# Kernel tuning notes

Hardware: AMD Instinct MI355X
Metric: run time of the kernel (lower is better)

Reference implementation:

```python
import jax, jax.numpy as jnp
import numpy as np

H, C = 4, 32
NT, NDAT, NDEV = 50000, 20000, 4
EDT, EVT, ETT = 800000, 200000, 400000


def _gat_conv(xs, xd, src, dst, ea, Ws, Wd, We, As, Ad, Ae, b, n_dst, concat):
    # linear projections -> [N, H, C]
    hs = (xs @ Ws).reshape(-1, H, C)
    hd = (xd @ Wd).reshape(-1, H, C)
    he = (ea @ We).reshape(-1, H, C)
    # per-edge attention logits [E, H]
    al = (hs * As).sum(-1)[src] + (hd * Ad).sum(-1)[dst] + (he * Ae).sum(-1)
    al = jax.nn.leaky_relu(al, 0.2)
    # segment softmax over incoming edges of each dst node
    amax = jax.ops.segment_max(al, dst, num_segments=n_dst)
    amax = jnp.where(jnp.isfinite(amax), amax, 0.0)
    ex = jnp.exp(al - amax[dst])
    den = jax.ops.segment_sum(ex, dst, num_segments=n_dst)
    w = ex / (den[dst] + 1e-16)
    # weighted scatter-add of source messages
    out = jax.ops.segment_sum(hs[src] * w[..., None], dst, num_segments=n_dst)
    out = out.reshape(n_dst, H * C) if concat else out.mean(axis=1)
    return out + b


def _add_self_loops_mean(src, dst, ea, n):
    # PyG add_self_loops(fill_value='mean'): loop edge_attr = mean of incoming edge_attr per node
    cnt = jax.ops.segment_sum(jnp.ones(dst.shape, ea.dtype), dst, num_segments=n)
    ea_mean = jax.ops.segment_sum(ea, dst, num_segments=n) / jnp.maximum(cnt, 1.0)[:, None]
    loops = jnp.arange(n, dtype=src.dtype)
    return (jnp.concatenate([src, loops]), jnp.concatenate([dst, loops]),
            jnp.concatenate([ea, ea_mean], axis=0))


def setup_inputs() -> dict:
    key = jax.random.key(0)
    ks = iter(jax.random.split(key, 40))
    nrm = lambda shape, fan: jax.random.normal(next(ks), shape, jnp.float32) / np.sqrt(fan)
    inp = {}
    inp['x_data'] = jax.random.normal(next(ks), (NDAT, 8), jnp.float32)
    inp['x_tasks'] = jax.random.normal(next(ks), (NT, 16), jnp.float32)
    inp['x_dev'] = jax.random.normal(next(ks), (NDEV, 8), jnp.float32)
    inp['ei_dt'] = jnp.stack([jax.random.randint(next(ks), (EDT,), 0, NDAT),
                              jax.random.randint(next(ks), (EDT,), 0, NT)]).astype(jnp.int32)
    inp['ea_dt'] = jax.random.normal(next(ks), (EDT, 8), jnp.float32)
    inp['ei_vt'] = jnp.stack([jax.random.randint(next(ks), (EVT,), 0, NDEV),
                              jax.random.randint(next(ks), (EVT,), 0, NT)]).astype(jnp.int32)
    inp['ea_vt'] = jax.random.normal(next(ks), (EVT, 6), jnp.float32)
    inp['ei_tt'] = jnp.stack([jax.random.randint(next(ks), (ETT,), 0, NT),
                              jax.random.randint(next(ks), (ETT,), 0, NT)]).astype(jnp.int32)
    inp['ea_tt'] = jax.random.normal(next(ks), (ETT, 4), jnp.float32)
    # conv1: (data -> tasks), concat=True
    inp['Ws1'] = nrm((8, H * C), 8); inp['Wd1'] = nrm((16, H * C), 16); inp['We1'] = nrm((8, H * C), 8)
    inp['As1'] = nrm((H, C), C); inp['Ad1'] = nrm((H, C), C); inp['Ae1'] = nrm((H, C), C)
    inp['b1'] = jnp.zeros((H * C,), jnp.float32)
    # conv2: (devices -> tasks), concat=True
    inp['Ws2'] = nrm((8, H * C), 8); inp['Wd2'] = nrm((16, H * C), 16); inp['We2'] = nrm((6, H * C), 6)
    inp['As2'] = nrm((H, C), C); inp['Ad2'] = nrm((H, C), C); inp['Ae2'] = nrm((H, C), C)
    inp['b2'] = jnp.zeros((H * C,), jnp.float32)
    # conv3: tasks -> tasks, single lin (256 -> H*C), concat=False, self loops
    inp['W3'] = nrm((2 * H * C, H * C), 2 * H * C); inp['We3'] = nrm((4, H * C), 4)
    inp['As3'] = nrm((H, C), C); inp['Ad3'] = nrm((H, C), C); inp['Ae3'] = nrm((H, C), C)
    inp['b3'] = jnp.zeros((C,), jnp.float32)
    return inp


def reference(x_data, x_tasks, x_dev, ei_dt, ea_dt, ei_vt, ea_vt, ei_tt, ea_tt,
              Ws1, Wd1, We1, As1, Ad1, Ae1, b1,
              Ws2, Wd2, We2, As2, Ad2, Ae2, b2,
              W3, We3, As3, Ad3, Ae3, b3):
    t_data = jax.nn.relu(_gat_conv(x_data, x_tasks, ei_dt[0], ei_dt[1], ea_dt,
                                   Ws1, Wd1, We1, As1, Ad1, Ae1, b1, NT, True))
    t_dev = jax.nn.relu(_gat_conv(x_dev, x_tasks, ei_vt[0], ei_vt[1], ea_vt,
                                  Ws2, Wd2, We2, As2, Ad2, Ae2, b2, NT, True))
    tasks = jnp.concatenate([t_data, t_dev], axis=1)  # [NT, 256]
    src, dst, ea = _add_self_loops_mean(ei_tt[0], ei_tt[1], ea_tt, NT)
    x = _gat_conv(tasks, tasks, src, dst, ea, W3, W3, We3, As3, Ad3, Ae3, b3, NT, False)
    x = jax.nn.relu(x)
    # dropout(p=0.5) is identity in eval mode
    return x
```

## Files before the change

kernel.cpp:

```cpp
#include <hip/hip_runtime.h>
#include <math.h>

static const int NT = 50000, NDAT = 20000, NDEV = 4;
static const int EDT = 800000, EVT = 200000, ETT = 400000;

static const int SCAN_TILE = 2048, SCAN_NB = 25;

static const int HT   = EDT + EVT + ETT;
static const int IN_A = HT + NDAT * 128;
static const int IN_B = IN_A + NDAT * 4;
static const int IN_C = IN_B + NT * 4;
static const int IN_D = IN_C + NDEV * 128;
static const int IN_E = IN_D + NDEV * 4;
static const int IN_F = IN_E + 256 * 128;
static const int FRONT_N = IN_F;

static const size_t OFF_TASKS = 0;
static const size_t OFF_HS    = 12800000;
static const size_t OFF_RANK  = OFF_HS;
static const size_t OFF_HSB1  = OFF_HS + 1400000;
static const size_t OFF_REC1  = OFF_HS + 2680000;
static const size_t OFF_HSB3  = OFF_HS;
static const size_t OFF_REC2  = 19200000;
static const size_t OFF_REC3  = 20000000;
static const size_t OFF_DEG   = 23200000;
static const size_t OFF_RP    = 23350000;
static const size_t OFF_AS1   = 23500004;
static const size_t OFF_AD1   = 23580004;
static const size_t OFF_AD2   = 23780004;
static const size_t OFF_HS2   = 23980004;
static const size_t OFF_AS2   = 23980516;
static const size_t OFF_QS1   = 23980532;
static const size_t OFF_QD1   = 23980564;
static const size_t OFF_P1    = 23980628;
static const size_t OFF_QS2   = 23980660;
static const size_t OFF_QD2   = 23980692;
static const size_t OFF_P2    = 23980756;
static const size_t OFF_P3    = 23980780;
static const size_t OFF_BSUM  = 23980796;
static const size_t OFF_W3HT  = 23980924;
static const size_t OFF_W3LT  = 23997308;
static const size_t WS_TOTAL  = 24013692;

typedef short v8s __attribute__((ext_vector_type(8)));
typedef float v4f __attribute__((ext_vector_type(4)));

__device__ __forceinline__ float lrelu(float a) { return a > 0.f ? a : 0.2f * a; }
__device__ __forceinline__ unsigned short f2bf(float x) {
    unsigned int u = __float_as_uint(x);
    return (unsigned short)((u + 0x7FFFu + ((u >> 16) & 1u)) >> 16);
}
__device__ __forceinline__ float bf2f(unsigned short h) {
    return __uint_as_float(((unsigned int)h) << 16);
}
__device__ __forceinline__ float bfsel(unsigned int lo01, unsigned int lo23, int h) {
    unsigned int word = (h < 2) ? lo01 : lo23;
    return bf2f((unsigned short)((h & 1) ? (word >> 16) : (word & 0xFFFFu)));
}
__device__ __forceinline__ void cvt_split(const float4& A, const float4& B, v8s& hi, v8s& lo) {
    union { unsigned short u[8]; v8s v; } H, L;
    float f[8] = {A.x, A.y, A.z, A.w, B.x, B.y, B.z, B.w};
    #pragma unroll
    for (int i = 0; i < 8; ++i) {
        unsigned short h = f2bf(f[i]);
        H.u[i] = h;
        L.u[i] = f2bf(f[i] - bf2f(h));
    }
    hi = H.v; lo = L.v;
}

__global__ void k_proj_small(const float* Ws1, const float* As1,
                             const float* Wd1, const float* Ad1,
                             const float* We1, const float* Ae1,
                             const float* Ws2, const float* As2,
                             const float* Wd2, const float* Ad2,
                             const float* We2, const float* Ae2,
                             const float* We3, const float* Ae3,
                             float* Qs1, float* Qd1, float* P1,
                             float* Qs2, float* Qd2, float* P2, float* P3) {
    int t = threadIdx.x;
    const float *W, *A; float* O; int u;
    if      (t < 32)  { W = Ws1; A = As1; O = Qs1; u = t; }
    else if (t < 96)  { W = Wd1; A = Ad1; O = Qd1; u = t - 32; }
    else if (t < 128) { W = We1; A = Ae1; O = P1;  u = t - 96; }
    else if (t < 160) { W = Ws2; A = As2; O = Qs2; u = t - 128; }
    else if (t < 224) { W = Wd2; A = Ad2; O = Qd2; u = t - 160; }
    else if (t < 248) { W = We2; A = Ae2; O = P2;  u = t - 224; }
    else if (t < 264) { W = We3; A = Ae3; O = P3;  u = t - 248; }
    else return;
    int k = u >> 2, h = u & 3;
    float acc = 0.f;
    for (int c = 0; c < 32; ++c) acc += W[k * 128 + h * 32 + c] * A[h * 32 + c];
    O[k * 4 + h] = acc;
}

__global__ __launch_bounds__(256) void k_front(const float* __restrict__ x_data,
                                               const float* __restrict__ Ws1,
                                               unsigned short* __restrict__ hsb1,
                                               const float* __restrict__ Qs1,
                                               float* __restrict__ as1,
                                               const float* __restrict__ x_tasks,
                                               const float* __restrict__ Qd1,
                                               const float* __restrict__ Qd2,
                                               float* __restrict__ ad1, float* __restrict__ ad2,
                                               const float* __restrict__ x_dev,
                                               const float* __restrict__ Ws2,
                                               float* __restrict__ hs2,
                                               const float* __restrict__ Qs2,
                                               float* __restrict__ as2,
                                               const float* __restrict__ W3,
                                               unsigned short* __restrict__ w3hT,
                                               unsigned short* __restrict__ w3lT,
                                               const int* __restrict__ dt,
                                               const int* __restrict__ vt,
                                               const int* __restrict__ tt,
                                               int* __restrict__ deg,
                                               int* __restrict__ rank) {
    int idx = blockIdx.x * blockDim.x + threadIdx.x;
    if (idx < HT) {
        if (idx < EDT)
            rank[idx] = atomicAdd(&deg[dt[EDT + idx]], 1);
        else if (idx < EDT + EVT)
            rank[idx] = atomicAdd(&deg[NT + vt[EVT + (idx - EDT)]], 1);
        else
            rank[idx] = atomicAdd(&deg[2 * NT + tt[ETT + (idx - EDT - EVT)]], 1);
    } else if (idx < IN_A) {
        int i = idx - HT;
        int n = i >> 7, j = i & 127;
        float acc = 0.f;
        #pragma unroll
        for (int k = 0; k < 8; ++k) acc += x_data[n * 8 + k] * Ws1[k * 128 + j];
        hsb1[i] = f2bf(acc);
    } else if (idx < IN_B) {
        int i = idx - IN_A;
        int n = i >> 2, h = i & 3;
        float acc = 0.f;
        #pragma unroll
        for (int k = 0; k < 8; ++k) acc += x_data[n * 8 + k] * Qs1[k * 4 + h];
        as1[i] = acc;
    } else if (idx < IN_C) {
        int i = idx - IN_B;
        int n = i >> 2, h = i & 3;
        float a = 0.f, b = 0.f;
        #pragma unroll
        for (int k = 0; k < 16; ++k) {
            float v = x_tasks[n * 16 + k];
            a += v * Qd1[k * 4 + h];
            b += v * Qd2[k * 4 + h];
        }
        ad1[i] = a; ad2[i] = b;
    } else if (idx < IN_D) {
        int i = idx - IN_C;
        int n = i >> 7, j = i & 127;
        float acc = 0.f;
        #pragma unroll
        for (int k = 0; k < 8; ++k) acc += x_dev[n * 8 + k] * Ws2[k * 128 + j];
        hs2[i] = acc;
    } else if (idx < IN_E) {
        int i = idx - IN_D;
        int n = i >> 2, h = i & 3;
        float acc = 0.f;
        #pragma unroll
        for (int k = 0; k < 8; ++k) acc += x_dev[n * 8 + k] * Qs2[k * 4 + h];
        as2[i] = acc;
    } else if (idx < IN_F) {
        int i = idx - IN_E;
        int k = i >> 7, n = i & 127;
        float x = W3[i];
        unsigned short h = f2bf(x);
        w3hT[n * 256 + k] = h;
        w3lT[n * 256 + k] = f2bf(x - bf2f(h));
    }
}

__global__ __launch_bounds__(256) void k_scan_part(const int* __restrict__ deg,
                                                   int* __restrict__ bsum) {
    int b = blockIdx.x;
    int g = b / SCAN_NB, t = b % SCAN_NB;
    int base = t * SCAN_TILE + threadIdx.x * 8;
    const int* dg = deg + (size_t)g * NT;
    int s = 0;
    if (base + 8 <= NT) {
        int4 a = *reinterpret_cast<const int4*>(dg + base);
        int4 c = *reinterpret_cast<const int4*>(dg + base + 4);
        s = a.x + a.y + a.z + a.w + c.x + c.y + c.z + c.w;
    } else {
        for (int i = 0; i < 8; ++i) if (base + i < NT) s += dg[base + i];
    }
    __shared__ int red[256];
    red[threadIdx.x] = s;
    __syncthreads();
    for (int off = 128; off > 0; off >>= 1) {
        if (threadIdx.x < off) red[threadIdx.x] += red[threadIdx.x + off];
        __syncthreads();
    }
    if (threadIdx.x == 0) bsum[b] = red[0];
}

__global__ __launch_bounds__(256) void k_scan_final(const int* __restrict__ deg,
                                                    const int* __restrict__ bsum,
                                                    int* __restrict__ rp) {
    int b = blockIdx.x;
    int g = b / SCAN_NB, t = b % SCAN_NB;
    int tid = threadIdx.x;
    int base = t * SCAN_TILE + tid * 8;
    const int* dg = deg + (size_t)g * NT;
    int* rpg = rp + (size_t)g * (NT + 1);
    int v[8];
    int s = 0;
    if (base + 8 <= NT) {
        int4 a = *reinterpret_cast<const int4*>(dg + base);
        int4 c = *reinterpret_cast<const int4*>(dg + base + 4);
        v[0] = a.x; v[1] = a.y; v[2] = a.z; v[3] = a.w;
        v[4] = c.x; v[5] = c.y; v[6] = c.z; v[7] = c.w;
        s = v[0] + v[1] + v[2] + v[3] + v[4] + v[5] + v[6] + v[7];
    } else {
        #pragma unroll
        for (int i = 0; i < 8; ++i) {
            v[i] = (base + i < NT) ? dg[base + i] : 0;
            s += v[i];
        }
    }
    __shared__ int sums[256];
    sums[tid] = s;
    __syncthreads();
    for (int off = 1; off < 256; off <<= 1) {
        int x = (tid >= off) ? sums[tid - off] : 0;
        __syncthreads();
        sums[tid] += x;
        __syncthreads();
    }
    int toff = 0;
    for (int t2 = 0; t2 < t; ++t2) toff += bsum[g * SCAN_NB + t2];
    int run = toff + (tid ? sums[tid - 1] : 0);
    #pragma unroll
    for (int i = 0; i < 8; ++i) {
        int idx = base + i;
        if (idx < NT) {
            rpg[idx] = run; run += v[i];
            if (idx == NT - 1) rpg[NT] = run;
        }
    }
}

__global__ void k_permute_w(const int* __restrict__ dt, const int* __restrict__ vt,
                            const int* __restrict__ tt, const int* __restrict__ rank,
                            const int* __restrict__ rp,
                            const float* __restrict__ as1, const float* __restrict__ ad1,
                            const float* __restrict__ P1, const float* __restrict__ ea1,
                            const float* __restrict__ as2, const float* __restrict__ ad2,
                            const float* __restrict__ P2, const float* __restrict__ ea2,
                            const float* __restrict__ P3, const float* __restrict__ ea3,
                            uint4* __restrict__ rec1, uint4* __restrict__ rec2,
                            uint4* __restrict__ rec3) {
    int e = blockIdx.x * blockDim.x + threadIdx.x;
    if (e < EDT) {
        int s = dt[e], d = dt[EDT + e];
        int slot = rp[d] + rank[e];
        float l[4];
        #pragma unroll
        for (int h = 0; h < 4; ++h) l[h] = as1[s * 4 + h] + ad1[d * 4 + h];
        float4 A = *reinterpret_cast<const float4*>(&ea1[(size_t)e * 8]);
        float4 B = *reinterpret_cast<const float4*>(&ea1[(size_t)e * 8 + 4]);
        float ev[8] = {A.x, A.y, A.z, A.w, B.x, B.y, B.z, B.w};
        #pragma unroll
        for (int k = 0; k < 8; ++k)
            #pragma unroll
            for (int h = 0; h < 4; ++h) l[h] += ev[k] * P1[k * 4 + h];
        unsigned int w01 = (unsigned int)f2bf(expf(lrelu(l[0])))
                         | ((unsigned int)f2bf(expf(lrelu(l[1]))) << 16);
        unsigned int w23 = (unsigned int)f2bf(expf(lrelu(l[2])))
                         | ((unsigned int)f2bf(expf(lrelu(l[3]))) << 16);
        rec1[slot] = make_uint4(w01, w23, (unsigned int)s, 0u);
    } else if (e < EDT + EVT) {
        int ee = e - EDT;
        int s = vt[ee], d = vt[EVT + ee];
        int slot = rp[(NT + 1) + d] + rank[e];
        float l[4];
        #pragma unroll
        for (int h = 0; h < 4; ++h) l[h] = as2[s * 4 + h] + ad2[d * 4 + h];
        float2 a = *reinterpret_cast<const float2*>(&ea2[(size_t)ee * 6]);
        float2 b = *reinterpret_cast<const float2*>(&ea2[(size_t)ee * 6 + 2]);
        float2 c = *reinterpret_cast<const float2*>(&ea2[(size_t)ee * 6 + 4]);
        float ev[6] = {a.x, a.y, b.x, b.y, c.x, c.y};
        #pragma unroll
        for (int k = 0; k < 6; ++k)
            #pragma unroll
            for (int h = 0; h < 4; ++h) l[h] += ev[k] * P2[k * 4 + h];
        unsigned int w01 = (unsigned int)f2bf(expf(lrelu(l[0])))
                         | ((unsigned int)f2bf(expf(lrelu(l[1]))) << 16);
        unsigned int w23 = (unsigned int)f2bf(expf(lrelu(l[2])))
                         | ((unsigned int)f2bf(expf(lrelu(l[3]))) << 16);
        rec2[slot] = make_uint4(w01, w23, (unsigned int)s, 0u);
    } else if (e < EDT + EVT + ETT) {
        int ee = e - EDT - EVT;
        int s = tt[ee], d = tt[ETT + ee];
        int slot = rp[2 * (NT + 1) + d] + rank[e];
        float4 q = *reinterpret_cast<const float4*>(&ea3[(size_t)ee * 4]);
        float ae[4];
        #pragma unroll
        for (int h = 0; h < 4; ++h)
            ae[h] = q.x * P3[h] + q.y * P3[4 + h] + q.z * P3[8 + h] + q.w * P3[12 + h];
        unsigned int a01 = (unsigned int)f2bf(ae[0]) | ((unsigned int)f2bf(ae[1]) << 16);
        unsigned int a23 = (unsigned int)f2bf(ae[2]) | ((unsigned int)f2bf(ae[3]) << 16);
        rec3[slot] = make_uint4((unsigned int)s, a01, a23, 0u);
    }
}

__global__ __launch_bounds__(256) void k_gather12(const int* __restrict__ rp1,
                                                  const uint4* __restrict__ rec1,
                                                  const unsigned short* __restrict__ hsb,
                                                  const float* __restrict__ b1,
                                                  const int* __restrict__ rp2,
                                                  const uint4* __restrict__ rec2,
                                                  const float* __restrict__ hs2,
                                                  const float* __restrict__ b2,
                                                  float* __restrict__ tasks) {
    int tid = threadIdx.x;
    int lane = tid & 31;
    int h = lane >> 3;
    if (blockIdx.x < NT / 8) {
        int d = blockIdx.x * 8 + (tid >> 5);
        int c0 = (lane & 7) * 4;
        int i0 = rp1[d], i1 = rp1[d + 1];
        float a0 = 0.f, a1 = 0.f, a2 = 0.f, a3 = 0.f, den = 0.f;
        int i = i0;
        for (; i + 4 <= i1; i += 4) {
            uint4 r0 = rec1[i], r1 = rec1[i + 1], r2 = rec1[i + 2], r3 = rec1[i + 3];
            float w0 = bfsel(r0.x, r0.y, h);
            float w1 = bfsel(r1.x, r1.y, h);
            float w2 = bfsel(r2.x, r2.y, h);
            float w3 = bfsel(r3.x, r3.y, h);
            ushort4 m0 = *reinterpret_cast<const ushort4*>(&hsb[(size_t)r0.z * 128 + h * 32 + c0]);
            ushort4 m1 = *reinterpret_cast<const ushort4*>(&hsb[(size_t)r1.z * 128 + h * 32 + c0]);
            ushort4 m2 = *reinterpret_cast<const ushort4*>(&hsb[(size_t)r2.z * 128 + h * 32 + c0]);
            ushort4 m3 = *reinterpret_cast<const ushort4*>(&hsb[(size_t)r3.z * 128 + h * 32 + c0]);
            a0 += w0 * bf2f(m0.x) + w1 * bf2f(m1.x) + w2 * bf2f(m2.x) + w3 * bf2f(m3.x);
            a1 += w0 * bf2f(m0.y) + w1 * bf2f(m1.y) + w2 * bf2f(m2.y) + w3 * bf2f(m3.y);
            a2 += w0 * bf2f(m0.z) + w1 * bf2f(m1.z) + w2 * bf2f(m2.z) + w3 * bf2f(m3.z);
            a3 += w0 * bf2f(m0.w) + w1 * bf2f(m1.w) + w2 * bf2f(m2.w) + w3 * bf2f(m3.w);
            den += w0 + w1 + w2 + w3;
        }
        for (; i < i1; ++i) {
            uint4 r = rec1[i];
            float w = bfsel(r.x, r.y, h);
            ushort4 m = *reinterpret_cast<const ushort4*>(&hsb[(size_t)r.z * 128 + h * 32 + c0]);
            a0 += w * bf2f(m.x); a1 += w * bf2f(m.y);
            a2 += w * bf2f(m.z); a3 += w * bf2f(m.w);
            den += w;
        }
        int j0 = h * 32 + c0;
        float4 b4 = *reinterpret_cast<const float4*>(&b1[j0]);
        float r = 1.f / (den + 1e-16f);
        float4 o = make_float4(fmaxf(a0 * r + b4.x, 0.f), fmaxf(a1 * r + b4.y, 0.f),
                               fmaxf(a2 * r + b4.z, 0.f), fmaxf(a3 * r + b4.w, 0.f));
        *reinterpret_cast<float4*>(&tasks[(size_t)d * 256 + j0]) = o;
    } else {
        int d = (blockIdx.x - NT / 8) * 8 + (tid >> 5);
        int i0 = rp2[d], i1 = rp2[d + 1];
        float ax = 0.f, ay = 0.f, az = 0.f, aw = 0.f, den = 0.f;
        int i = i0;
        for (; i + 4 <= i1; i += 4) {
            uint4 r0 = rec2[i], r1 = rec2[i + 1], r2 = rec2[i + 2], r3 = rec2[i + 3];
            float w0 = bfsel(r0.x, r0.y, h);
            float w1 = bfsel(r1.x, r1.y, h);
            float w2 = bfsel(r2.x, r2.y, h);
            float w3 = bfsel(r3.x, r3.y, h);
            float4 v0 = *reinterpret_cast<const float4*>(&hs2[r0.z * 128 + lane * 4]);
            float4 v1 = *reinterpret_cast<const float4*>(&hs2[r1.z * 128 + lane * 4]);
            float4 v2 = *reinterpret_cast<const float4*>(&hs2[r2.z * 128 + lane * 4]);
            float4 v3 = *reinterpret_cast<const float4*>(&hs2[r3.z * 128 + lane * 4]);
            ax += v0.x * w0 + v1.x * w1 + v2.x * w2 + v3.x * w3;
            ay += v0.y * w0 + v1.y * w1 + v2.y * w2 + v3.y * w3;
            az += v0.z * w0 + v1.z * w1 + v2.z * w2 + v3.z * w3;
            aw += v0.w * w0 + v1.w * w1 + v2.w * w2 + v3.w * w3;
            den += w0 + w1 + w2 + w3;
        }
        for (; i < i1; ++i) {
            uint4 r4 = rec2[i];
            float w = bfsel(r4.x, r4.y, h);
            float4 v = *reinterpret_cast<const float4*>(&hs2[r4.z * 128 + lane * 4]);
            ax += v.x * w; ay += v.y * w; az += v.z * w; aw += v.w * w;
            den += w;
        }
        float4 b4 = *reinterpret_cast<const float4*>(&b2[lane * 4]);
        float r = 1.f / (den + 1e-16f);
        float4 o = make_float4(fmaxf(ax * r + b4.x, 0.f), fmaxf(ay * r + b4.y, 0.f),
                               fmaxf(az * r + b4.z, 0.f), fmaxf(aw * r + b4.w, 0.f));
        *reinterpret_cast<float4*>(&tasks[(size_t)d * 256 + 128 + lane * 4]) = o;
    }
}

__global__ __launch_bounds__(256) void k_gather_c3(const int* __restrict__ rp,
                                                   const uint4* __restrict__ rec,
                                                   const float* __restrict__ as3,
                                                   const float* __restrict__ ad3,
                                                   const unsigned short* __restrict__ hsb,
                                                   const float* __restrict__ b3,
                                                   float* __restrict__ out) {
    int tid = threadIdx.x;
    int d = blockIdx.x * 8 + (tid >> 5);
    int lane = tid & 31;
    int h = lane >> 3;
    int c0 = (lane & 7) * 4;
    float adv = ad3[d * 4 + h];
    int i0 = rp[d], i1 = rp[d + 1];
    float a0 = 0.f, a1 = 0.f, a2 = 0.f, a3 = 0.f, den = 0.f, aes = 0.f;
    int i = i0;
    for (; i + 4 <= i1; i += 4) {
        uint4 r0 = rec[i], r1 = rec[i + 1], r2 = rec[i + 2], r3 = rec[i + 3];
        float s0 = as3[(size_t)r0.x * 4 + h], s1 = as3[(size_t)r1.x * 4 + h];
        float s2 = as3[(size_t)r2.x * 4 + h], s3 = as3[(size_t)r3.x * 4 + h];
        ushort4 m0 = *reinterpret_cast<const ushort4*>(&hsb[(size_t)r0.x * 128 + h * 32 + c0]);
        ushort4 m1 = *reinterpret_cast<const ushort4*>(&hsb[(size_t)r1.x * 128 + h * 32 + c0]);
        ushort4 m2 = *reinterpret_cast<const ushort4*>(&hsb[(size_t)r2.x * 128 + h * 32 + c0]);
        ushort4 m3 = *reinterpret_cast<const ushort4*>(&hsb[(size_t)r3.x * 128 + h * 32 + c0]);
        float ae0 = bfsel(r0.y, r0.z, h);
        float ae1 = bfsel(r1.y, r1.z, h);
        float ae2 = bfsel(r2.y, r2.z, h);
        float ae3 = bfsel(r3.y, r3.z, h);
        float w0 = expf(lrelu(s0 + adv + ae0));
        float w1 = expf(lrelu(s1 + adv + ae1));
        float w2 = expf(lrelu(s2 + adv + ae2));
        float w3 = expf(lrelu(s3 + adv + ae3));
        a0 += w0 * bf2f(m0.x) + w1 * bf2f(m1.x) + w2 * bf2f(m2.x) + w3 * bf2f(m3.x);
        a1 += w0 * bf2f(m0.y) + w1 * bf2f(m1.y) + w2 * bf2f(m2.y) + w3 * bf2f(m3.y);
        a2 += w0 * bf2f(m0.z) + w1 * bf2f(m1.z) + w2 * bf2f(m2.z) + w3 * bf2f(m3.z);
        a3 += w0 * bf2f(m0.w) + w1 * bf2f(m1.w) + w2 * bf2f(m2.w) + w3 * bf2f(m3.w);
        den += w0 + w1 + w2 + w3;
        aes += ae0 + ae1 + ae2 + ae3;
    }
    for (; i < i1; ++i) {
        uint4 r4 = rec[i];
        float s = as3[(size_t)r4.x * 4 + h];
        ushort4 m = *reinterpret_cast<const ushort4*>(&hsb[(size_t)r4.x * 128 + h * 32 + c0]);
        float ae = bfsel(r4.y, r4.z, h);
        float w = expf(lrelu(s + adv + ae));
        a0 += w * bf2f(m.x); a1 += w * bf2f(m.y);
        a2 += w * bf2f(m.z); a3 += w * bf2f(m.w);
        den += w; aes += ae;
    }
    float cnt = (float)(i1 - i0);
    float mloop = aes / fmaxf(cnt, 1.f);
    float exl = expf(lrelu(as3[(size_t)d * 4 + h] + adv + mloop));
    ushort4 md = *reinterpret_cast<const ushort4*>(&hsb[(size_t)d * 128 + h * 32 + c0]);
    float rden = 1.f / (den + exl + 1e-16f);
    float p0 = (a0 + exl * bf2f(md.x)) * rden;
    float p1 = (a1 + exl * bf2f(md.y)) * rden;
    float p2 = (a2 + exl * bf2f(md.z)) * rden;
    float p3 = (a3 + exl * bf2f(md.w)) * rden;
    p0 += __shfl_xor(p0, 8, 32); p0 += __shfl_xor(p0, 16, 32);
    p1 += __shfl_xor(p1, 8, 32); p1 += __shfl_xor(p1, 16, 32);
    p2 += __shfl_xor(p2, 8, 32); p2 += __shfl_xor(p2, 16, 32);
    p3 += __shfl_xor(p3, 8, 32); p3 += __shfl_xor(p3, 16, 32);
    if ((lane >> 3) == 0) {
        float4 o;
        o.x = fmaxf(0.25f * p0 + b3[c0 + 0], 0.f);
        o.y = fmaxf(0.25f * p1 + b3[c0 + 1], 0.f);
        o.z = fmaxf(0.25f * p2 + b3[c0 + 2], 0.f);
        o.w = fmaxf(0.25f * p3 + b3[c0 + 3], 0.f);
        *reinterpret_cast<float4*>(&out[(size_t)d * 32 + c0]) = o;
    }
}

__global__ __launch_bounds__(256, 2) void k_gemm_mfma(const float* __restrict__ T,
                                                      const unsigned short* __restrict__ w3hT,
                                                      const unsigned short* __restrict__ w3lT,
                                                      const float* __restrict__ As3,
                                                      const float* __restrict__ Ad3,
                                                      unsigned short* __restrict__ hsb,
                                                      float* __restrict__ as3o,
                                                      float* __restrict__ ad3o) {
    __shared__ uint4 sB[2][2048];
    int tid = threadIdx.x;
    int lane = tid & 63;
    int arow = lane & 15;
    int kgrp = lane >> 4;
    int s0 = blockIdx.x * 8 + (tid >> 6) * 2;
    int ss0 = s0 < 3125 ? s0 : 3124;
    int ss1 = (s0 + 1) < 3125 ? (s0 + 1) : 3124;
    const uint4* w3h4 = reinterpret_cast<const uint4*>(w3hT);
    const uint4* w3l4 = reinterpret_cast<const uint4*>(w3lT);

    v4f acc[2][8];
    #pragma unroll
    for (int sp = 0; sp < 2; ++sp)
        #pragma unroll
        for (int nt = 0; nt < 8; ++nt) acc[sp][nt] = (v4f)0.f;

    #pragma unroll
    for (int kt = 0; kt < 2; ++kt) {
        __syncthreads();
        float4 a0[8], a1[8];
        const float* Ta0 = T + (size_t)(ss0 * 16 + arow) * 256 + kt * 128 + kgrp * 8;
        const float* Ta1 = T + (size_t)(ss1 * 16 + arow) * 256 + kt * 128 + kgrp * 8;
        #pragma unroll
        for (int kc = 0; kc < 4; ++kc) {
            a0[kc * 2]     = *reinterpret_cast<const float4*>(Ta0 + kc * 32);
            a0[kc * 2 + 1] = *reinterpret_cast<const float4*>(Ta0 + kc * 32 + 4);
            a1[kc * 2]     = *reinterpret_cast<const float4*>(Ta1 + kc * 32);
            a1[kc * 2 + 1] = *reinterpret_cast<const float4*>(Ta1 + kc * 32 + 4);
        }
        #pragma unroll
        for (int it = 0; it < 8; ++it) {
            int c = it * 256 + tid;
            int n = c >> 4, ch = c & 15;
            int gi = n * 32 + kt * 16 + ch;
            int li = n * 16 + (ch ^ (n & 7));
            sB[0][li] = w3h4[gi];
            sB[1][li] = w3l4[gi];
        }
        __syncthreads();
        #pragma unroll
        for (int kc = 0; kc < 4; ++kc) {
            v8s ah0, al0, ah1, al1;
            cvt_split(a0[kc * 2], a0[kc * 2 + 1], ah0, al0);
            cvt_split(a1[kc * 2], a1[kc * 2 + 1], ah1, al1);
            #pragma unroll
            for (int nt = 0; nt < 8; ++nt) {
                int col = nt * 16 + arow;
                int ch = kc * 4 + kgrp;
                int li = col * 16 + (ch ^ (col & 7));
                v8s bh = *reinterpret_cast<const v8s*>(&sB[0][li]);
                v8s bl = *reinterpret_cast<const v8s*>(&sB[1][li]);
                acc[0][nt] = __builtin_amdgcn_mfma_f32_16x16x32_bf16(ah0, bh, acc[0][nt], 0, 0, 0);
                acc[0][nt] = __builtin_amdgcn_mfma_f32_16x16x32_bf16(ah0, bl, acc[0][nt], 0, 0, 0);
                acc[0][nt] = __builtin_amdgcn_mfma_f32_16x16x32_bf16(al0, bh, acc[0][nt], 0, 0, 0);
                acc[1][nt] = __builtin_amdgcn_mfma_f32_16x16x32_bf16(ah1, bh, acc[1][nt], 0, 0, 0);
                acc[1][nt] = __builtin_amdgcn_mfma_f32_16x16x32_bf16(ah1, bl, acc[1][nt], 0, 0, 0);
                acc[1][nt] = __builtin_amdgcn_mfma_f32_16x16x32_bf16(al1, bh, acc[1][nt], 0, 0, 0);
            }
        }
    }
    float As3v[8], Ad3v[8];
    #pragma unroll
    for (int nt = 0; nt < 8; ++nt) {
        As3v[nt] = As3[nt * 16 + arow];
        Ad3v[nt] = Ad3[nt * 16 + arow];
    }
    #pragma unroll
    for (int sp = 0; sp < 2; ++sp) {
        int s = s0 + sp;
        if (s >= 3125) continue;
        #pragma unroll
        for (int i = 0; i < 4; ++i) {
            int row = s * 16 + kgrp * 4 + i;
            #pragma unroll
            for (int nt = 0; nt < 8; ++nt)
                hsb[(size_t)row * 128 + nt * 16 + arow] = f2bf(acc[sp][nt][i]);
            #pragma unroll
            for (int h = 0; h < 4; ++h) {
                float pa = acc[sp][2 * h][i] * As3v[2 * h] + acc[sp][2 * h + 1][i] * As3v[2 * h + 1];
                float pb = acc[sp][2 * h][i] * Ad3v[2 * h] + acc[sp][2 * h + 1][i] * Ad3v[2 * h + 1];
                #pragma unroll
                for (int off = 1; off < 16; off <<= 1) {
                    pa += __shfl_xor(pa, off, 64);
                    pb += __shfl_xor(pb, off, 64);
                }
                if (arow == 0) {
                    as3o[row * 4 + h] = pa;
                    ad3o[row * 4 + h] = pb;
                }
            }
        }
    }
}

extern "C" void kernel_launch(void* const* d_in, const int* in_sizes, int n_in,
                              void* d_out, int out_size, void* d_ws, size_t ws_size,
                              hipStream_t stream) {
    const float* x_data  = (const float*)d_in[0];
    const float* x_tasks = (const float*)d_in[1];
    const float* x_dev   = (const float*)d_in[2];
    const int*   ei_dt   = (const int*)d_in[3];
    const float* ea_dt   = (const float*)d_in[4];
    const int*   ei_vt   = (const int*)d_in[5];
    const float* ea_vt   = (const float*)d_in[6];
    const int*   ei_tt   = (const int*)d_in[7];
    const float* ea_tt   = (const float*)d_in[8];
    const float* Ws1 = (const float*)d_in[9];  const float* Wd1 = (const float*)d_in[10];
    const float* We1 = (const float*)d_in[11]; const float* As1 = (const float*)d_in[12];
    const float* Ad1 = (const float*)d_in[13]; const float* Ae1 = (const float*)d_in[14];
    const float* b1  = (const float*)d_in[15];
    const float* Ws2 = (const float*)d_in[16]; const float* Wd2 = (const float*)d_in[17];
    const float* We2 = (const float*)d_in[18]; const float* As2 = (const float*)d_in[19];
    const float* Ad2 = (const float*)d_in[20]; const float* Ae2 = (const float*)d_in[21];
    const float* b2  = (const float*)d_in[22];
    const float* W3  = (const float*)d_in[23]; const float* We3 = (const float*)d_in[24];
    const float* As3 = (const float*)d_in[25]; const float* Ad3 = (const float*)d_in[26];
    const float* Ae3 = (const float*)d_in[27]; const float* b3  = (const float*)d_in[28];

    if (ws_size < WS_TOTAL * sizeof(float)) return;

    float* w = (float*)d_ws;
    float* tasks = w + OFF_TASKS;
    int*   rank  = (int*)(w + OFF_RANK);
    unsigned short* hsb1 = (unsigned short*)(w + OFF_HSB1);
    unsigned short* hsb3 = (unsigned short*)(w + OFF_HSB3);
    uint4* rec1  = (uint4*)(w + OFF_REC1);
    uint4* rec2  = (uint4*)(w + OFF_REC2);
    uint4* rec3  = (uint4*)(w + OFF_REC3);
    int*   deg   = (int*)(w + OFF_DEG);
    int*   rp    = (int*)(w + OFF_RP);
    int*   bsum  = (int*)(w + OFF_BSUM);
    unsigned short* w3hT = (unsigned short*)(w + OFF_W3HT);
    unsigned short* w3lT = (unsigned short*)(w + OFF_W3LT);
    float* as1 = w + OFF_AS1;
    float* ad1 = w + OFF_AD1; float* as3 = w + OFF_AD1;
    float* ad2 = w + OFF_AD2; float* ad3 = w + OFF_AD2;
    float* hs2 = w + OFF_HS2; float* as2 = w + OFF_AS2;
    float* Qs1 = w + OFF_QS1; float* Qd1 = w + OFF_QD1; float* P1 = w + OFF_P1;
    float* Qs2 = w + OFF_QS2; float* Qd2 = w + OFF_QD2; float* P2 = w + OFF_P2;
    float* P3  = w + OFF_P3;
    float* out = (float*)d_out;

    dim3 B(256);
    #define GRID(n) dim3((unsigned)(((n) + 255) / 256))

    hipMemsetAsync(deg, 0, 3 * NT * sizeof(int), stream);
    k_proj_small<<<1, 320, 0, stream>>>(Ws1, As1, Wd1, Ad1, We1, Ae1,
                                        Ws2, As2, Wd2, Ad2, We2, Ae2, We3, Ae3,
                                        Qs1, Qd1, P1, Qs2, Qd2, P2, P3);
    k_front<<<GRID(FRONT_N), B, 0, stream>>>(x_data, Ws1, hsb1, Qs1, as1,
                                             x_tasks, Qd1, Qd2, ad1, ad2,
                                             x_dev, Ws2, hs2, Qs2, as2,
                                             W3, w3hT, w3lT,
                                             ei_dt, ei_vt, ei_tt, deg, rank);
    k_scan_part<<<dim3(3 * SCAN_NB), B, 0, stream>>>(deg, bsum);
    k_scan_final<<<dim3(3 * SCAN_NB), B, 0, stream>>>(deg, bsum, rp);
    k_permute_w<<<GRID(EDT + EVT + ETT), B, 0, stream>>>(ei_dt, ei_vt, ei_tt, rank, rp,
                                                         as1, ad1, P1, ea_dt,
                                                         as2, ad2, P2, ea_vt,
                                                         P3, ea_tt,
                                                         rec1, rec2, rec3);
    k_gather12<<<dim3(2 * (NT / 8)), B, 0, stream>>>(rp, rec1, hsb1, b1,
                                                     rp + (NT + 1), rec2, hs2, b2, tasks);
    k_gemm_mfma<<<dim3(391), dim3(256), 0, stream>>>(tasks, w3hT, w3lT, As3, Ad3,
                                                     hsb3, as3, ad3);
    k_gather_c3<<<dim3(NT / 8), B, 0, stream>>>(rp + 2 * (NT + 1), rec3, as3, ad3,
                                                hsb3, b3, out);
    #undef GRID
}
```

Baseline: 215.5 us.

## Privatize degree counters per XCD to cut cross-die atomic contention

Replaces the single set of per-node degree counters with eight copies, one per XCD. The XCD id is read from a hardware register, and the counters are bumped with workgroup-scope relaxed atomics. The XCD id is packed into the rank, and the scan now sums all eight copies and writes per-XCD base offsets back into the counters. The permute step then computes each slot from the right XCD's base. The aim is to keep the edge-counting atomics in the local L2 instead of contending across dies, in exchange for eight times the counter memory, a larger memset, and more scan reads and writes.

```diff
diff --git a/kernel.cpp b/kernel.cpp
--- a/kernel.cpp
+++ b/kernel.cpp
@@ -5,6 +5,7 @@
 static const int EDT = 800000, EVT = 200000, ETT = 400000;
 
 static const int SCAN_TILE = 2048, SCAN_NB = 25;
+static const int DEG_STRIDE = 3 * NT;
 
 static const int HT   = EDT + EVT + ETT;
 static const int IN_A = HT + NDAT * 128;
@@ -23,7 +24,7 @@
 static const size_t OFF_HSB3  = OFF_HS;
 static const size_t OFF_REC2  = 19200000;
 static const size_t OFF_REC3  = 20000000;
-static const size_t OFF_DEG   = 23200000;
+static const size_t OFF_DEG8  = 21600000;
 static const size_t OFF_RP    = 23350000;
 static const size_t OFF_AS1   = 23500004;
 static const size_t OFF_AD1   = 23580004;
@@ -114,16 +115,28 @@
                                                const int* __restrict__ dt,
                                                const int* __restrict__ vt,
                                                const int* __restrict__ tt,
-                                               int* __restrict__ deg,
+                                               int* __restrict__ deg8,
                                                int* __restrict__ rank) {
     int idx = blockIdx.x * blockDim.x + threadIdx.x;
     if (idx < HT) {
-        if (idx < EDT)
-            rank[idx] = atomicAdd(&deg[dt[EDT + idx]], 1);
-        else if (idx < EDT + EVT)
-            rank[idx] = atomicAdd(&deg[NT + vt[EVT + (idx - EDT)]], 1);
-        else
-            rank[idx] = atomicAdd(&deg[2 * NT + tt[ETT + (idx - EDT - EVT)]], 1);
+        unsigned int xcc;
+        asm volatile("s_getreg_b32 %0, hwreg(20, 0, 32)" : "=s"(xcc));
+        xcc &= 7u;
+        int* dg = deg8 + (size_t)xcc * DEG_STRIDE;
+        int r;
+        if (idx < EDT) {
+            r = __hip_atomic_fetch_add(&dg[dt[EDT + idx]], 1,
+                                       __ATOMIC_RELAXED, __HIP_MEMORY_SCOPE_WORKGROUP);
+            rank[idx] = (r << 3) | (int)xcc;
+        } else if (idx < EDT + EVT) {
+            r = __hip_atomic_fetch_add(&dg[NT + vt[EVT + (idx - EDT)]], 1,
+                                       __ATOMIC_RELAXED, __HIP_MEMORY_SCOPE_WORKGROUP);
+            rank[idx] = (r << 3) | (int)xcc;
+        } else {
+            r = __hip_atomic_fetch_add(&dg[2 * NT + tt[ETT + (idx - EDT - EVT)]], 1,
+                                       __ATOMIC_RELAXED, __HIP_MEMORY_SCOPE_WORKGROUP);
+            rank[idx] = (r << 3) | (int)xcc;
+        }
     } else if (idx < IN_A) {
         int i = idx - HT;
         int n = i >> 7, j = i & 127;
@@ -173,19 +186,23 @@
     }
 }
 
-__global__ __launch_bounds__(256) void k_scan_part(const int* __restrict__ deg,
+__global__ __launch_bounds__(256) void k_scan_part(const int* __restrict__ deg8,
                                                    int* __restrict__ bsum) {
     int b = blockIdx.x;
     int g = b / SCAN_NB, t = b % SCAN_NB;
     int base = t * SCAN_TILE + threadIdx.x * 8;
-    const int* dg = deg + (size_t)g * NT;
+    const int* dg = deg8 + (size_t)g * NT;
     int s = 0;
-    if (base + 8 <= NT) {
-        int4 a = *reinterpret_cast<const int4*>(dg + base);
-        int4 c = *reinterpret_cast<const int4*>(dg + base + 4);
-        s = a.x + a.y + a.z + a.w + c.x + c.y + c.z + c.w;
-    } else {
-        for (int i = 0; i < 8; ++i) if (base + i < NT) s += dg[base + i];
+    #pragma unroll
+    for (int x = 0; x < 8; ++x) {
+        const int* dx = dg + (size_t)x * DEG_STRIDE;
+        if (base + 8 <= NT) {
+            int4 a = *reinterpret_cast<const int4*>(dx + base);
+            int4 c = *reinterpret_cast<const int4*>(dx + base + 4);
+            s += a.x + a.y + a.z + a.w + c.x + c.y + c.z + c.w;
+        } else {
+            for (int i = 0; i < 8; ++i) if (base + i < NT) s += dx[base + i];
+        }
     }
     __shared__ int red[256];
     red[threadIdx.x] = s;
@@ -197,29 +214,28 @@
     if (threadIdx.x == 0) bsum[b] = red[0];
 }
 
-__global__ __launch_bounds__(256) void k_scan_final(const int* __restrict__ deg,
+__global__ __launch_bounds__(256) void k_scan_final(int* __restrict__ deg8,
                                                     const int* __restrict__ bsum,
                                                     int* __restrict__ rp) {
     int b = blockIdx.x;
     int g = b / SCAN_NB, t = b % SCAN_NB;
     int tid = threadIdx.x;
     int base = t * SCAN_TILE + tid * 8;
-    const int* dg = deg + (size_t)g * NT;
+    int* dg = deg8 + (size_t)g * NT;
     int* rpg = rp + (size_t)g * (NT + 1);
+    int c[8][8];
     int v[8];
     int s = 0;
-    if (base + 8 <= NT) {
-        int4 a = *reinterpret_cast<const int4*>(dg + base);
-        int4 c = *reinterpret_cast<const int4*>(dg + base + 4);
-        v[0] = a.x; v[1] = a.y; v[2] = a.z; v[3] = a.w;
-        v[4] = c.x; v[5] = c.y; v[6] = c.z; v[7] = c.w;
-        s = v[0] + v[1] + v[2] + v[3] + v[4] + v[5] + v[6] + v[7];
-    } else {
-        #pragma unroll
-        for (int i = 0; i < 8; ++i) {
-            v[i] = (base + i < NT) ? dg[base + i] : 0;
-            s += v[i];
-        }
+    #pragma unroll
+    for (int i = 0; i < 8; ++i) {
+        int idx = base + i;
+        int tot = 0;
+        #pragma unroll
+        for (int x = 0; x < 8; ++x) {
+            int val = (idx < NT) ? dg[(size_t)x * DEG_STRIDE + idx] : 0;
+            c[i][x] = val; tot += val;
+        }
+        v[i] = tot; s += tot;
     }
     __shared__ int sums[256];
     sums[tid] = s;
@@ -237,7 +253,14 @@
     for (int i = 0; i < 8; ++i) {
         int idx = base + i;
         if (idx < NT) {
-            rpg[idx] = run; run += v[i];
+            rpg[idx] = run;
+            int bb = run;
+            #pragma unroll
+            for (int x = 0; x < 8; ++x) {
+                dg[(size_t)x * DEG_STRIDE + idx] = bb;
+                bb += c[i][x];
+            }
+            run += v[i];
             if (idx == NT - 1) rpg[NT] = run;
         }
     }
@@ -245,7 +268,7 @@
 
 __global__ void k_permute_w(const int* __restrict__ dt, const int* __restrict__ vt,
                             const int* __restrict__ tt, const int* __restrict__ rank,
-                            const int* __restrict__ rp,
+                            const int* __restrict__ base8,
                             const float* __restrict__ as1, const float* __restrict__ ad1,
                             const float* __restrict__ P1, const float* __restrict__ ea1,
                             const float* __restrict__ as2, const float* __restrict__ ad2,
@@ -256,7 +279,8 @@
     int e = blockIdx.x * blockDim.x + threadIdx.x;
     if (e < EDT) {
         int s = dt[e], d = dt[EDT + e];
-        int slot = rp[d] + rank[e];
+        int rk = rank[e];
+        int slot = base8[(size_t)(rk & 7) * DEG_STRIDE + d] + (rk >> 3);
         float l[4];
         #pragma unroll
         for (int h = 0; h < 4; ++h) l[h] = as1[s * 4 + h] + ad1[d * 4 + h];
@@ -275,7 +299,8 @@
     } else if (e < EDT + EVT) {
         int ee = e - EDT;
         int s = vt[ee], d = vt[EVT + ee];
-        int slot = rp[(NT + 1) + d] + rank[e];
+        int rk = rank[e];
+        int slot = base8[(size_t)(rk & 7) * DEG_STRIDE + NT + d] + (rk >> 3);
         float l[4];
         #pragma unroll
         for (int h = 0; h < 4; ++h) l[h] = as2[s * 4 + h] + ad2[d * 4 + h];
@@ -295,7 +320,8 @@
     } else if (e < EDT + EVT + ETT) {
         int ee = e - EDT - EVT;
         int s = tt[ee], d = tt[ETT + ee];
-        int slot = rp[2 * (NT + 1) + d] + rank[e];
+        int rk = rank[e];
+        int slot = base8[(size_t)(rk & 7) * DEG_STRIDE + 2 * NT + d] + (rk >> 3);
         float4 q = *reinterpret_cast<const float4*>(&ea3[(size_t)ee * 4]);
         float ae[4];
         #pragma unroll
@@ -600,7 +626,7 @@
     uint4* rec1  = (uint4*)(w + OFF_REC1);
     uint4* rec2  = (uint4*)(w + OFF_REC2);
     uint4* rec3  = (uint4*)(w + OFF_REC3);
-    int*   deg   = (int*)(w + OFF_DEG);
+    int*   deg8  = (int*)(w + OFF_DEG8);
     int*   rp    = (int*)(w + OFF_RP);
     int*   bsum  = (int*)(w + OFF_BSUM);
     unsigned short* w3hT = (unsigned short*)(w + OFF_W3HT);
@@ -617,7 +643,7 @@
     dim3 B(256);
     #define GRID(n) dim3((unsigned)(((n) + 255) / 256))
 
-    hipMemsetAsync(deg, 0, 3 * NT * sizeof(int), stream);
+    hipMemsetAsync(deg8, 0, 8 * DEG_STRIDE * sizeof(int), stream);
     k_proj_small<<<1, 320, 0, stream>>>(Ws1, As1, Wd1, Ad1, We1, Ae1,
                                         Ws2, As2, Wd2, Ad2, We2, Ae2, We3, Ae3,
                                         Qs1, Qd1, P1, Qs2, Qd2, P2, P3);
@@ -625,10 +651,10 @@
                                              x_tasks, Qd1, Qd2, ad1, ad2,
                                              x_dev, Ws2, hs2, Qs2, as2,
                                              W3, w3hT, w3lT,
-                                             ei_dt, ei_vt, ei_tt, deg, rank);
-    k_scan_part<<<dim3(3 * SCAN_NB), B, 0, stream>>>(deg, bsum);
-    k_scan_final<<<dim3(3 * SCAN_NB), B, 0, stream>>>(deg, bsum, rp);
-    k_permute_w<<<GRID(EDT + EVT + ETT), B, 0, stream>>>(ei_dt, ei_vt, ei_tt, rank, rp,
+                                             ei_dt, ei_vt, ei_tt, deg8, rank);
+    k_scan_part<<<dim3(3 * SCAN_NB), B, 0, stream>>>(deg8, bsum);
+    k_scan_final<<<dim3(3 * SCAN_NB), B, 0, stream>>>(deg8, bsum, rp);
+    k_permute_w<<<GRID(EDT + EVT + ETT), B, 0, stream>>>(ei_dt, ei_vt, ei_tt, rank, deg8,
                                                          as1, ad1, P1, ea_dt,
                                                          as2, ad2, P2, ea_vt,
                                                          P3, ea_tt,
```

After: 223.9 us. 1.04x slower.
